# Kernel optimization log

Hardware: AMD Instinct MI355X
Metric: run time of the kernel (lower is better)

## Reference

```python
import jax, jax.numpy as jnp
import numpy as np

B = 500_000
D = 128
L = 4


def setup_inputs() -> dict:
    key = jax.random.key(0)
    k1, k2 = jax.random.split(key)
    inputs = jax.random.normal(k1, (B, D), dtype=jnp.float32)
    # xavier_normal for [D,1] slices: std = sqrt(2/(D+1))
    std = float(np.sqrt(2.0 / (D + 1)))
    kernels = jax.random.normal(k2, (L, D, 1), dtype=jnp.float32) * std
    biases = jnp.zeros((L, D, 1), dtype=jnp.float32)
    return {"inputs": inputs, "kernels": kernels, "biases": biases}


def reference(inputs, kernels, biases):
    # inputs: [B, D]; kernels/biases: [L, D, 1]
    x0 = inputs  # [B, D]
    xl = x0
    for i in range(kernels.shape[0]):
        w = kernels[i, :, 0]  # [D]
        b = biases[i, :, 0]   # [D]
        xl_w = jnp.einsum('bd,d->b', xl, w)  # [B], scalar per sample
        xl = x0 * xl_w[:, None] + b + xl     # rank-1 cross + bias + residual
    return xl
```

## Files before the change

kernel.cpp:

```cpp
#include <hip/hip_runtime.h>


#define CN_D 128
#define CN_L 4

__global__ __launch_bounds__(256) void crossnet_kernel(
    const float* __restrict__ inputs,
    const float* __restrict__ kernels,
    const float* __restrict__ biases,
    float* __restrict__ out,
    int nrows)
{
    const int lane = threadIdx.x & 31;
    const int row_in_blk = threadIdx.x >> 5;
    const int rows_per_blk = blockDim.x >> 5;

    float4 w4[CN_L], b4[CN_L];
#pragma unroll
    for (int i = 0; i < CN_L; ++i) {
        w4[i] = ((const float4*)(kernels + i * CN_D))[lane];
        b4[i] = ((const float4*)(biases + i * CN_D))[lane];
    }

    for (long long row = (long long)blockIdx.x * rows_per_blk + row_in_blk;
         row < nrows;
         row += (long long)gridDim.x * rows_per_blk)
    {
        const float4* xp = (const float4*)(inputs + row * CN_D);
        float4 x = xp[lane];
        float4 xl = x;

#pragma unroll
        for (int i = 0; i < CN_L; ++i) {
            float p = xl.x * w4[i].x + xl.y * w4[i].y
                    + xl.z * w4[i].z + xl.w * w4[i].w;
            p += __shfl_xor(p, 1);
            p += __shfl_xor(p, 2);
            p += __shfl_xor(p, 4);
            p += __shfl_xor(p, 8);
            p += __shfl_xor(p, 16);
            xl.x = fmaf(x.x, p, xl.x + b4[i].x);
            xl.y = fmaf(x.y, p, xl.y + b4[i].y);
            xl.z = fmaf(x.z, p, xl.z + b4[i].z);
            xl.w = fmaf(x.w, p, xl.w + b4[i].w);
        }

        float4* op = (float4*)(out + row * CN_D);
        op[lane] = xl;
    }
}

extern "C" void kernel_launch(void* const* d_in, const int* in_sizes, int n_in,
                              void* d_out, int out_size, void* d_ws, size_t ws_size,
                              hipStream_t stream) {
    const float* inputs  = (const float*)d_in[0];
    const float* kernels = (const float*)d_in[1];
    const float* biases  = (const float*)d_in[2];
    float* out = (float*)d_out;

    const int nrows = in_sizes[0] / CN_D;

    const int block = 256;
    const int grid  = 4096;

    crossnet_kernel<<<grid, block, 0, stream>>>(inputs, kernels, biases, out, nrows);
}
```

Baseline: 418.3 us.

## Collapse cross layers into scalar recurrence with 8-lane rows and nontemporal stores

```diff
diff --git a/kernel.cpp b/kernel.cpp
--- a/kernel.cpp
+++ b/kernel.cpp
@@ -1,52 +1,90 @@
 #include <hip/hip_runtime.h>
 
+
+typedef float vf4 __attribute__((ext_vector_type(4)));
 
 #define CN_D 128
 #define CN_L 4
 
-__global__ __launch_bounds__(256) void crossnet_kernel(
+__device__ __forceinline__ float dot4(vf4 a, vf4 b) {
+    return fmaf(a.x, b.x, fmaf(a.y, b.y, fmaf(a.z, b.z, a.w * b.w)));
+}
+
+__device__ __forceinline__ vf4 fma4s(vf4 x, float c, vf4 d) {
+    vf4 r;
+    r.x = fmaf(x.x, c, d.x);
+    r.y = fmaf(x.y, c, d.y);
+    r.z = fmaf(x.z, c, d.z);
+    r.w = fmaf(x.w, c, d.w);
+    return r;
+}
+
+__global__ __launch_bounds__(256, 4) void crossnet_kernel(
     const float* __restrict__ inputs,
     const float* __restrict__ kernels,
     const float* __restrict__ biases,
     float* __restrict__ out,
     int nrows)
 {
-    const int lane = threadIdx.x & 31;
-    const int row_in_blk = threadIdx.x >> 5;
-    const int rows_per_blk = blockDim.x >> 5;
+    const int j   = threadIdx.x & 7;
+    const int grp = threadIdx.x >> 3;
+    const int rows_per_blk = blockDim.x >> 3;
 
-    float4 w4[CN_L], b4[CN_L];
+    vf4 w[CN_L][4];
 #pragma unroll
-    for (int i = 0; i < CN_L; ++i) {
-        w4[i] = ((const float4*)(kernels + i * CN_D))[lane];
-        b4[i] = ((const float4*)(biases + i * CN_D))[lane];
+    for (int i = 0; i < CN_L; ++i)
+#pragma unroll
+        for (int k = 0; k < 4; ++k)
+            w[i][k] = ((const vf4*)(kernels + i * CN_D))[j + 8 * k];
+
+    float u[CN_L];
+    u[0] = 0.f;
+    vf4 d[4];
+#pragma unroll
+    for (int k = 0; k < 4; ++k)
+        d[k] = ((const vf4*)(biases))[j + 8 * k];
+#pragma unroll
+    for (int i = 1; i < CN_L; ++i) {
+        float p = dot4(w[i][0], d[0]) + dot4(w[i][1], d[1])
+                + dot4(w[i][2], d[2]) + dot4(w[i][3], d[3]);
+        p += __shfl_xor(p, 1);
+        p += __shfl_xor(p, 2);
+        p += __shfl_xor(p, 4);
+        u[i] = p;
+#pragma unroll
+        for (int k = 0; k < 4; ++k)
+            d[k] += ((const vf4*)(biases + i * CN_D))[j + 8 * k];
     }
 
-    for (long long row = (long long)blockIdx.x * rows_per_blk + row_in_blk;
+    for (long long row = (long long)blockIdx.x * rows_per_blk + grp;
          row < nrows;
          row += (long long)gridDim.x * rows_per_blk)
     {
-        const float4* xp = (const float4*)(inputs + row * CN_D);
-        float4 x = xp[lane];
-        float4 xl = x;
+        const vf4* xp = (const vf4*)(inputs + row * CN_D);
+        vf4 x0 = xp[j];
+        vf4 x1 = xp[j + 8];
+        vf4 x2 = xp[j + 16];
+        vf4 x3 = xp[j + 24];
 
-#pragma unroll
-        for (int i = 0; i < CN_L; ++i) {
-            float p = xl.x * w4[i].x + xl.y * w4[i].y
-                    + xl.z * w4[i].z + xl.w * w4[i].w;
-            p += __shfl_xor(p, 1);
-            p += __shfl_xor(p, 2);
-            p += __shfl_xor(p, 4);
-            p += __shfl_xor(p, 8);
-            p += __shfl_xor(p, 16);
-            xl.x = fmaf(x.x, p, xl.x + b4[i].x);
-            xl.y = fmaf(x.y, p, xl.y + b4[i].y);
-            xl.z = fmaf(x.z, p, xl.z + b4[i].z);
-            xl.w = fmaf(x.w, p, xl.w + b4[i].w);
-        }
+        float t0 = dot4(x0, w[0][0]) + dot4(x1, w[0][1]) + dot4(x2, w[0][2]) + dot4(x3, w[0][3]);
+        float t1 = dot4(x0, w[1][0]) + dot4(x1, w[1][1]) + dot4(x2, w[1][2]) + dot4(x3, w[1][3]);
+        float t2 = dot4(x0, w[2][0]) + dot4(x1, w[2][1]) + dot4(x2, w[2][2]) + dot4(x3, w[2][3]);
+        float t3 = dot4(x0, w[3][0]) + dot4(x1, w[3][1]) + dot4(x2, w[3][2]) + dot4(x3, w[3][3]);
 
-        float4* op = (float4*)(out + row * CN_D);
-        op[lane] = xl;
+        t0 += __shfl_xor(t0, 1); t1 += __shfl_xor(t1, 1); t2 += __shfl_xor(t2, 1); t3 += __shfl_xor(t3, 1);
+        t0 += __shfl_xor(t0, 2); t1 += __shfl_xor(t1, 2); t2 += __shfl_xor(t2, 2); t3 += __shfl_xor(t3, 2);
+        t0 += __shfl_xor(t0, 4); t1 += __shfl_xor(t1, 4); t2 += __shfl_xor(t2, 4); t3 += __shfl_xor(t3, 4);
+
+        float c = 1.f + t0;
+        c = fmaf(c, t1, c) + u[1];
+        c = fmaf(c, t2, c) + u[2];
+        c = fmaf(c, t3, c) + u[3];
+
+        vf4* op = (vf4*)(out + row * CN_D);
+        __builtin_nontemporal_store(fma4s(x0, c, d[0]), &op[j]);
+        __builtin_nontemporal_store(fma4s(x1, c, d[1]), &op[j + 8]);
+        __builtin_nontemporal_store(fma4s(x2, c, d[2]), &op[j + 16]);
+        __builtin_nontemporal_store(fma4s(x3, c, d[3]), &op[j + 24]);
     }
 }
 
@@ -61,7 +99,8 @@
     const int nrows = in_sizes[0] / CN_D;
 
     const int block = 256;
-    const int grid  = 4096;
+    long long nblk = ((long long)nrows + 31) / 32;
+    const int grid = (int)(nblk < 2048 ? nblk : 2048);
 
     crossnet_kernel<<<grid, block, 0, stream>>>(inputs, kernels, biases, out, nrows);
 }
```

Result: slower. 433.1 us (+3.5%).
